# Kernel tuning notes

Hardware: AMD Instinct MI355X
Metric: run time of the kernel (lower is better)

Reference implementation:

```python
import jax, jax.numpy as jnp
import numpy as np

B, H, E_DIM, V = 512, 2048, 1024, 50257


def setup_inputs() -> dict:
    key = jax.random.key(0)
    ks = jax.random.split(key, 10)
    s_e = 1.0 / np.sqrt(E_DIM)
    s_h = 1.0 / np.sqrt(H)
    return {
        "inp": jax.random.randint(ks[0], (B,), 0, V),
        "h_0": jax.random.normal(ks[1], (B, H), jnp.float32) * 0.1,
        "c_0": jax.random.normal(ks[2], (B, H), jnp.float32) * 0.1,
        "E": jax.random.normal(ks[3], (V, E_DIM), jnp.float32),
        "Wx": jax.random.normal(ks[4], (4, H, E_DIM), jnp.float32) * s_e,
        "bx": jax.random.normal(ks[5], (4, H), jnp.float32) * s_e,
        "Wh": jax.random.normal(ks[6], (4, H, H), jnp.float32) * s_h,
        "bh": jax.random.normal(ks[7], (4, H), jnp.float32) * s_h,
        "Wd": jax.random.normal(ks[8], (V, H), jnp.float32) * s_h,
        "bd": jax.random.normal(ks[9], (V,), jnp.float32) * s_h,
    }


def reference(inp, h_0, c_0, E, Wx, bx, Wh, bh, Wd, bd):
    # Embedding lookup: [B, E_DIM]
    x = E[inp]
    # Two fused GEMMs for all 4 gates (gate order: f, i, o, c): [B, 4, H]
    gates = (jnp.einsum('be,ghe->bgh', x, Wx) + bx[None]
             + jnp.einsum('bh,gkh->bgk', h_0, Wh) + bh[None])
    f_g = jax.nn.sigmoid(gates[:, 0])
    i_g = jax.nn.sigmoid(gates[:, 1])
    o_g = jax.nn.sigmoid(gates[:, 2])
    c_tilda = jnp.tanh(gates[:, 3])
    cx = f_g * c_0 + i_g * c_tilda
    hx = o_g * jnp.tanh(cx)
    out = hx @ Wd.T + bd  # [B, V]
    return out, hx, cx
```

## Files before the change

### kernel.cpp

```cpp
#include <hip/hip_runtime.h>
#include <hip/hip_bf16.h>

using bf16x8 = __attribute__((ext_vector_type(8))) short;
using f32x4  = __attribute__((ext_vector_type(4))) float;

#define DEVI __device__ __forceinline__

DEVI unsigned short bf16r(float f)
{
    return __builtin_bit_cast(unsigned short, __float2bfloat16(f));
}

DEVI bf16x8 cvt8(const f32x4 a, const f32x4 b)
{
    bf16x8 r;
#pragma unroll
    for (int j = 0; j < 4; ++j) {
        r[j]     = (short)bf16r(a[j]);
        r[4 + j] = (short)bf16r(b[j]);
    }
    return r;
}

__global__ __launch_bounds__(256) void k_gather(const float* __restrict__ E,
                                                const int* __restrict__ inp,
                                                unsigned short* __restrict__ x)
{
    const int b = blockIdx.x;
    const long r = inp[b];
    const f32x4 v = ((const f32x4*)(E + r * 1024L))[threadIdx.x];
    ushort4 o;
    o.x = bf16r(v[0]); o.y = bf16r(v[1]); o.z = bf16r(v[2]); o.w = bf16r(v[3]);
    ((ushort4*)(x + (long)b * 1024L))[threadIdx.x] = o;
}

__global__ __launch_bounds__(256) void k_cvtn(const float* __restrict__ in,
                                              unsigned short* __restrict__ out)
{
    const long i = (blockIdx.x * 256L + threadIdx.x) * 8;
    const f32x4 a = *(const f32x4*)(in + i);
    const f32x4 b = *(const f32x4*)(in + i + 4);
    *(bf16x8*)(out + i) = cvt8(a, b);
}


DEVI bf16x8 lds_frag(const char* lds, int row, int j)
{
    return *(const bf16x8*)(lds + row * 128 + ((j ^ (row & 7)) << 4));
}

DEVI void mfma_tile8(const char* sA, const char* sB, int l, int wr, int wc,
                     f32x4 (&acc)[4][4])
{
#pragma unroll
    for (int ks = 0; ks < 2; ++ks) {
        bf16x8 af[4], bq[4];
#pragma unroll
        for (int m = 0; m < 4; ++m)
            af[m] = lds_frag(sA, wr * 64 + m * 16 + (l & 15), ks * 4 + (l >> 4));
#pragma unroll
        for (int n = 0; n < 4; ++n)
            bq[n] = lds_frag(sB, wc * 64 + n * 16 + (l & 15), ks * 4 + (l >> 4));
#pragma unroll
        for (int m = 0; m < 4; ++m)
#pragma unroll
            for (int n = 0; n < 4; ++n)
                acc[m][n] = __builtin_amdgcn_mfma_f32_16x16x32_bf16(
                    af[m], bq[n], acc[m][n], 0, 0, 0);
    }
}

template <bool CLAMP>
DEVI void gemm_core8(const unsigned short* __restrict__ A, long lda, long arow0,
                     const float* __restrict__ B, long ldb, long brow0, long bmax,
                     int nt, long kbase, int t, char* lds, f32x4 (&acc)[4][4])
{
    char* sA0 = lds;
    char* sA1 = lds + 32768;
    char* sB0 = lds + 65536;
    char* sB1 = lds + 81920;
    const int l = t & 63, w = t >> 6, wr = w >> 1, wc = w & 1;

    const unsigned short* ap[4];
    int aswz[4];
#pragma unroll
    for (int i = 0; i < 4; ++i) {
        const int g = i * 512 + t, row = g >> 3, j = g & 7;
        ap[i] = A + (arow0 + row) * lda + kbase + j * 8;
        aswz[i] = row * 128 + ((j ^ (row & 7)) << 4);
    }
    const float* bp[2];
    int bswz[2];
#pragma unroll
    for (int i = 0; i < 2; ++i) {
        const int g = i * 512 + t, row = g >> 3, j = g & 7;
        long br = brow0 + row;
        if (CLAMP) br = (br < bmax) ? br : (bmax - 1);
        bp[i] = B + br * ldb + kbase + j * 8;
        bswz[i] = row * 128 + ((j ^ (row & 7)) << 4);
    }

    bf16x8 ra0[4], ra1[4];
    f32x4 rb0[4], rb1[4];

#define LOADR(as, bs)                                                          \
    do {                                                                       \
        _Pragma("unroll") for (int i = 0; i < 4; ++i) {                        \
            as[i] = *(const bf16x8*)ap[i];                                     \
            ap[i] += 64;                                                       \
        }                                                                      \
        _Pragma("unroll") for (int i = 0; i < 2; ++i) {                        \
            bs[2 * i]     = *(const f32x4*)bp[i];                              \
            bs[2 * i + 1] = *(const f32x4*)(bp[i] + 4);                        \
            bp[i] += 64;                                                       \
        }                                                                      \
    } while (0)
#define WRLDS(sa, sb, as, bs)                                                  \
    do {                                                                       \
        _Pragma("unroll") for (int i = 0; i < 4; ++i)                          \
            *(bf16x8*)((sa) + aswz[i]) = as[i];                                \
        _Pragma("unroll") for (int i = 0; i < 2; ++i)                          \
            *(bf16x8*)((sb) + bswz[i]) = cvt8(bs[2 * i], bs[2 * i + 1]);       \
    } while (0)
#define WAITV8  asm volatile("s_waitcnt vmcnt(8)" ::: "memory")
#define WAITV0  asm volatile("s_waitcnt vmcnt(0)" ::: "memory")
#define WAITL0  asm volatile("s_waitcnt lgkmcnt(0)" ::: "memory")
#define BARRIER __builtin_amdgcn_s_barrier()

    LOADR(ra0, rb0);
    LOADR(ra1, rb1);
    WAITV8;
    WRLDS(sA0, sB0, ra0, rb0);
    LOADR(ra0, rb0);
    WAITL0; BARRIER;

    for (int kt = 0; kt < nt; kt += 2) {
        if (kt + 2 < nt) WAITV8; else WAITV0;
        WRLDS(sA1, sB1, ra1, rb1);
        if (kt + 3 < nt) LOADR(ra1, rb1);
        mfma_tile8(sA0, sB0, l, wr, wc, acc);
        WAITL0; BARRIER;
        if (kt + 2 < nt) {
            if (kt + 3 < nt) WAITV8; else WAITV0;
            WRLDS(sA0, sB0, ra0, rb0);
            if (kt + 4 < nt) LOADR(ra0, rb0);
        }
        mfma_tile8(sA1, sB1, l, wr, wc, acc);
        WAITL0; BARRIER;
    }
#undef LOADR
#undef WRLDS
#undef WAITV8
#undef WAITV0
#undef WAITL0
#undef BARRIER
}

__global__ __launch_bounds__(512, 2) void k_gates(
    const unsigned short* __restrict__ xb, const float* __restrict__ Wx,
    const unsigned short* __restrict__ h0b, const float* __restrict__ Wh,
    float* __restrict__ g0, float* __restrict__ g1, float* __restrict__ g2)
{
    extern __shared__ __align__(16) char lds[];
    const int t = threadIdx.x;
    const int bid = blockIdx.x;
    const int xcd = bid & 7, slot = bid >> 3;
    const int L = xcd * 48 + slot;
    const int z = L >> 7;
    const int mtile = L & 1;
    const int ntile = (L >> 1) & 63;

    const unsigned short* A; const float* B; long lda, ldb, kbase; float* C; int nt;
    if (z == 0)      { A = xb;  lda = 1024; B = Wx; ldb = 1024; kbase = 0;    C = g0; nt = 16; }
    else if (z == 1) { A = h0b; lda = 2048; B = Wh; ldb = 2048; kbase = 0;    C = g1; nt = 16; }
    else             { A = h0b; lda = 2048; B = Wh; ldb = 2048; kbase = 1024; C = g2; nt = 16; }

    f32x4 acc[4][4] = {};
    gemm_core8<false>(A, lda, (long)mtile * 256, B, ldb, (long)ntile * 128,
                      1L << 40, nt, kbase, t, lds, acc);

    const int l = t & 63, w = t >> 6, wr = w >> 1, wc = w & 1;
    const int lc = l & 15, r4 = (l >> 4) * 4;
#pragma unroll
    for (int n = 0; n < 4; ++n) {
        const long col = (long)ntile * 128 + wc * 64 + n * 16 + lc;
#pragma unroll
        for (int m = 0; m < 4; ++m) {
            const long row = (long)mtile * 256 + wr * 64 + m * 16 + r4;
#pragma unroll
            for (int r = 0; r < 4; ++r)
                C[(row + r) * 8192 + col] = acc[m][n][r];
        }
    }
}

__global__ __launch_bounds__(512, 2) void k_dec(
    const unsigned short* __restrict__ hxb, const float* __restrict__ Wd,
    const float* __restrict__ bd, float* __restrict__ out)
{
    extern __shared__ __align__(16) char lds[];
    const int t = threadIdx.x;
    const int bid = blockIdx.x;
    const int xcd = bid & 7, slot = bid >> 3;
    const int L = (xcd < 2) ? (xcd * 99 + slot) : (198 + (xcd - 2) * 98 + slot);
    const int mtile = L & 1;
    const int ntile = L >> 1;
    const long N = 50257;

    f32x4 acc[4][4] = {};
    gemm_core8<true>(hxb, 2048, (long)mtile * 256, Wd, 2048, (long)ntile * 128,
                     N, 32, 0, t, lds, acc);

    const int l = t & 63, w = t >> 6, wr = w >> 1, wc = w & 1;
    const int lc = l & 15, r4 = (l >> 4) * 4;
#pragma unroll
    for (int n = 0; n < 4; ++n) {
        const long col = (long)ntile * 128 + wc * 64 + n * 16 + lc;
        if (col >= N) continue;
        const float bias = bd[col];
#pragma unroll
        for (int m = 0; m < 4; ++m) {
            const long row = (long)mtile * 256 + wr * 64 + m * 16 + r4;
#pragma unroll
            for (int r = 0; r < 4; ++r)
                out[(row + r) * N + col] = acc[m][n][r] + bias;
        }
    }
}

__global__ __launch_bounds__(256) void k_lstm(
    const float* __restrict__ g0, const float* __restrict__ g1,
    const float* __restrict__ g2, const float* __restrict__ bx,
    const float* __restrict__ bh, const float* __restrict__ c0,
    float* __restrict__ hx, float* __restrict__ cx,
    unsigned short* __restrict__ hxb)
{
    const int i = blockIdx.x * 256 + threadIdx.x;
    const int b = i >> 9;
    const int hc = (i & 511) << 2;
    const long base = (long)b * 8192;

    f32x4 g[4];
#pragma unroll
    for (int gi = 0; gi < 4; ++gi) {
        const long off = base + gi * 2048 + hc;
        const int boff = gi * 2048 + hc;
        g[gi] = *(const f32x4*)(g0 + off);
        g[gi] += *(const f32x4*)(g1 + off);
        g[gi] += *(const f32x4*)(g2 + off);
        g[gi] += *(const f32x4*)(bx + boff);
        g[gi] += *(const f32x4*)(bh + boff);
    }
    const f32x4 c0v = *(const f32x4*)(c0 + (long)b * 2048 + hc);

    f32x4 cv, hv;
    ushort4 hb;
#pragma unroll
    for (int j = 0; j < 4; ++j) {
        const float fg = 1.f / (1.f + __expf(-g[0][j]));
        const float ig = 1.f / (1.f + __expf(-g[1][j]));
        const float og = 1.f / (1.f + __expf(-g[2][j]));
        const float e2 = __expf(2.f * g[3][j]);
        const float ct = 1.f - 2.f / (e2 + 1.f);
        const float c  = fg * c0v[j] + ig * ct;
        const float e2c = __expf(2.f * c);
        const float th  = 1.f - 2.f / (e2c + 1.f);
        cv[j] = c;
        hv[j] = og * th;
    }
    hb.x = bf16r(hv[0]); hb.y = bf16r(hv[1]); hb.z = bf16r(hv[2]); hb.w = bf16r(hv[3]);

    const long o = (long)b * 2048 + hc;
    *(f32x4*)(cx + o) = cv;
    *(f32x4*)(hx + o) = hv;
    *(ushort4*)(hxb + o) = hb;
}

extern "C" void kernel_launch(void* const* d_in, const int* in_sizes, int n_in,
                              void* d_out, int out_size, void* d_ws, size_t ws_size,
                              hipStream_t stream)
{
    const int*   inp = (const int*)d_in[0];
    const float* h0  = (const float*)d_in[1];
    const float* c0  = (const float*)d_in[2];
    const float* E   = (const float*)d_in[3];
    const float* Wx  = (const float*)d_in[4];
    const float* bx  = (const float*)d_in[5];
    const float* Wh  = (const float*)d_in[6];
    const float* bh  = (const float*)d_in[7];
    const float* Wd  = (const float*)d_in[8];
    const float* bd  = (const float*)d_in[9];

    float* out = (float*)d_out;
    float* hx  = out + 512L * 50257L;
    float* cx  = hx + 512L * 2048L;

    unsigned short* xb  = (unsigned short*)out;
    float* g0 = out + (1L << 20);
    float* g1 = out + (5L << 20);
    float* g2 = out + (9L << 20);
    unsigned short* h0b = (unsigned short*)(out + (13L << 20));
    unsigned short* hxb = (unsigned short*)d_ws;

    k_gather<<<512, 256, 0, stream>>>(E, inp, xb);
    k_cvtn<<<512, 256, 0, stream>>>(h0, h0b);

    k_gates<<<384, 512, 98304, stream>>>(xb, Wx, h0b, Wh, g0, g1, g2);

    k_lstm<<<1024, 256, 0, stream>>>(g0, g1, g2, bx, bh, c0, hx, cx, hxb);

    k_dec<<<786, 512, 98304, stream>>>(hxb, Wd, bd, out);
}
```

Baseline: 284.8 us.

## Use full-M 512-row tiles with K=32 steps so weights are read once

The GEMM core now covers all 512 batch rows in one block with 128 columns, using a K step of 32 instead of 64. Each weight row is therefore loaded from HBM and converted to bf16 only once, where before it was loaded twice across two M tiles. This roughly halves the dominant fp32 weight traffic for the decoder and gate GEMMs. The cost is half as many blocks (393 decoder blocks, 192 gate blocks), a larger accumulator that drops the two-blocks-per-CU launch bound, smaller K steps that double the number of barriers, and removal of the XCD-aware block remapping.

```diff
diff --git a/kernel.cpp b/kernel.cpp
--- a/kernel.cpp
+++ b/kernel.cpp
@@ -44,119 +44,109 @@
 }
 
 
-DEVI bf16x8 lds_frag(const char* lds, int row, int j)
-{
-    return *(const bf16x8*)(lds + row * 128 + ((j ^ (row & 7)) << 4));
-}
-
-DEVI void mfma_tile8(const char* sA, const char* sB, int l, int wr, int wc,
-                     f32x4 (&acc)[4][4])
-{
-#pragma unroll
-    for (int ks = 0; ks < 2; ++ks) {
-        bf16x8 af[4], bq[4];
-#pragma unroll
-        for (int m = 0; m < 4; ++m)
-            af[m] = lds_frag(sA, wr * 64 + m * 16 + (l & 15), ks * 4 + (l >> 4));
+DEVI void mfma_tile512(const char* sA, const char* sB, int l, int wr, int wc,
+                       f32x4 (&acc)[8][4])
+{
+    const int j = l >> 4;
+    bf16x8 af[8], bq[4];
+#pragma unroll
+    for (int m = 0; m < 8; ++m) {
+        const int row = wr * 128 + m * 16 + (l & 15);
+        af[m] = *(const bf16x8*)(sA + row * 64 + ((j ^ (row & 3)) << 4));
+    }
+#pragma unroll
+    for (int n = 0; n < 4; ++n) {
+        const int row = wc * 64 + n * 16 + (l & 15);
+        bq[n] = *(const bf16x8*)(sB + row * 64 + ((j ^ (row & 3)) << 4));
+    }
+#pragma unroll
+    for (int m = 0; m < 8; ++m)
 #pragma unroll
         for (int n = 0; n < 4; ++n)
-            bq[n] = lds_frag(sB, wc * 64 + n * 16 + (l & 15), ks * 4 + (l >> 4));
-#pragma unroll
-        for (int m = 0; m < 4; ++m)
-#pragma unroll
-            for (int n = 0; n < 4; ++n)
-                acc[m][n] = __builtin_amdgcn_mfma_f32_16x16x32_bf16(
-                    af[m], bq[n], acc[m][n], 0, 0, 0);
-    }
+            acc[m][n] = __builtin_amdgcn_mfma_f32_16x16x32_bf16(
+                af[m], bq[n], acc[m][n], 0, 0, 0);
 }
 
 template <bool CLAMP>
-DEVI void gemm_core8(const unsigned short* __restrict__ A, long lda, long arow0,
-                     const float* __restrict__ B, long ldb, long brow0, long bmax,
-                     int nt, long kbase, int t, char* lds, f32x4 (&acc)[4][4])
+DEVI void gemm_core512(const unsigned short* __restrict__ A, long lda,
+                       const float* __restrict__ B, long ldb, long bcol0,
+                       long bmax, int nt, long kbase, int t, char* lds,
+                       f32x4 (&acc)[8][4])
 {
     char* sA0 = lds;
     char* sA1 = lds + 32768;
     char* sB0 = lds + 65536;
-    char* sB1 = lds + 81920;
+    char* sB1 = lds + 73728;
     const int l = t & 63, w = t >> 6, wr = w >> 1, wc = w & 1;
 
     const unsigned short* ap[4];
     int aswz[4];
 #pragma unroll
     for (int i = 0; i < 4; ++i) {
-        const int g = i * 512 + t, row = g >> 3, j = g & 7;
-        ap[i] = A + (arow0 + row) * lda + kbase + j * 8;
-        aswz[i] = row * 128 + ((j ^ (row & 7)) << 4);
-    }
-    const float* bp[2];
-    int bswz[2];
-#pragma unroll
-    for (int i = 0; i < 2; ++i) {
-        const int g = i * 512 + t, row = g >> 3, j = g & 7;
-        long br = brow0 + row;
-        if (CLAMP) br = (br < bmax) ? br : (bmax - 1);
-        bp[i] = B + br * ldb + kbase + j * 8;
-        bswz[i] = row * 128 + ((j ^ (row & 7)) << 4);
-    }
+        const int g = i * 512 + t, row = g >> 2, j = g & 3;
+        ap[i] = A + row * lda + kbase + j * 8;
+        aswz[i] = row * 64 + ((j ^ (row & 3)) << 4);
+    }
+    const int brow = t >> 2, bseg = t & 3;
+    long br = bcol0 + brow;
+    if (CLAMP) br = (br < bmax) ? br : (bmax - 1);
+    const float* bp = B + br * ldb + kbase + bseg * 8;
+    const int bswz = brow * 64 + ((bseg ^ (brow & 3)) << 4);
 
     bf16x8 ra0[4], ra1[4];
-    f32x4 rb0[4], rb1[4];
+    f32x4 rb0[2], rb1[2];
 
 #define LOADR(as, bs)                                                          \
     do {                                                                       \
         _Pragma("unroll") for (int i = 0; i < 4; ++i) {                        \
             as[i] = *(const bf16x8*)ap[i];                                     \
-            ap[i] += 64;                                                       \
+            ap[i] += 32;                                                       \
         }                                                                      \
-        _Pragma("unroll") for (int i = 0; i < 2; ++i) {                        \
-            bs[2 * i]     = *(const f32x4*)bp[i];                              \
-            bs[2 * i + 1] = *(const f32x4*)(bp[i] + 4);                        \
-            bp[i] += 64;                                                       \
-        }                                                                      \
+        bs[0] = *(const f32x4*)bp;                                             \
+        bs[1] = *(const f32x4*)(bp + 4);                                       \
+        bp += 32;                                                              \
     } while (0)
 #define WRLDS(sa, sb, as, bs)                                                  \
     do {                                                                       \
         _Pragma("unroll") for (int i = 0; i < 4; ++i)                          \
             *(bf16x8*)((sa) + aswz[i]) = as[i];                                \
-        _Pragma("unroll") for (int i = 0; i < 2; ++i)                          \
-            *(bf16x8*)((sb) + bswz[i]) = cvt8(bs[2 * i], bs[2 * i + 1]);       \
+        *(bf16x8*)((sb) + bswz) = cvt8(bs[0], bs[1]);                          \
     } while (0)
-#define WAITV8  asm volatile("s_waitcnt vmcnt(8)" ::: "memory")
+#define WAITV6  asm volatile("s_waitcnt vmcnt(6)" ::: "memory")
 #define WAITV0  asm volatile("s_waitcnt vmcnt(0)" ::: "memory")
 #define WAITL0  asm volatile("s_waitcnt lgkmcnt(0)" ::: "memory")
 #define BARRIER __builtin_amdgcn_s_barrier()
 
     LOADR(ra0, rb0);
     LOADR(ra1, rb1);
-    WAITV8;
+    WAITV6;
     WRLDS(sA0, sB0, ra0, rb0);
     LOADR(ra0, rb0);
     WAITL0; BARRIER;
 
     for (int kt = 0; kt < nt; kt += 2) {
-        if (kt + 2 < nt) WAITV8; else WAITV0;
+        if (kt + 2 < nt) WAITV6; else WAITV0;
         WRLDS(sA1, sB1, ra1, rb1);
         if (kt + 3 < nt) LOADR(ra1, rb1);
-        mfma_tile8(sA0, sB0, l, wr, wc, acc);
+        mfma_tile512(sA0, sB0, l, wr, wc, acc);
         WAITL0; BARRIER;
         if (kt + 2 < nt) {
-            if (kt + 3 < nt) WAITV8; else WAITV0;
+            if (kt + 3 < nt) WAITV6; else WAITV0;
             WRLDS(sA0, sB0, ra0, rb0);
             if (kt + 4 < nt) LOADR(ra0, rb0);
         }
-        mfma_tile8(sA1, sB1, l, wr, wc, acc);
+        mfma_tile512(sA1, sB1, l, wr, wc, acc);
         WAITL0; BARRIER;
     }
 #undef LOADR
 #undef WRLDS
-#undef WAITV8
+#undef WAITV6
 #undef WAITV0
 #undef WAITL0
 #undef BARRIER
 }
 
-__global__ __launch_bounds__(512, 2) void k_gates(
+__global__ __launch_bounds__(512) void k_gates(
     const unsigned short* __restrict__ xb, const float* __restrict__ Wx,
     const unsigned short* __restrict__ h0b, const float* __restrict__ Wh,
     float* __restrict__ g0, float* __restrict__ g1, float* __restrict__ g2)
@@ -164,20 +154,17 @@
     extern __shared__ __align__(16) char lds[];
     const int t = threadIdx.x;
     const int bid = blockIdx.x;
-    const int xcd = bid & 7, slot = bid >> 3;
-    const int L = xcd * 48 + slot;
-    const int z = L >> 7;
-    const int mtile = L & 1;
-    const int ntile = (L >> 1) & 63;
-
-    const unsigned short* A; const float* B; long lda, ldb, kbase; float* C; int nt;
-    if (z == 0)      { A = xb;  lda = 1024; B = Wx; ldb = 1024; kbase = 0;    C = g0; nt = 16; }
-    else if (z == 1) { A = h0b; lda = 2048; B = Wh; ldb = 2048; kbase = 0;    C = g1; nt = 16; }
-    else             { A = h0b; lda = 2048; B = Wh; ldb = 2048; kbase = 1024; C = g2; nt = 16; }
-
-    f32x4 acc[4][4] = {};
-    gemm_core8<false>(A, lda, (long)mtile * 256, B, ldb, (long)ntile * 128,
-                      1L << 40, nt, kbase, t, lds, acc);
+    const int z = bid >> 6;
+    const int ntile = bid & 63;
+
+    const unsigned short* A; const float* B; long lda, ldb, kbase; float* C;
+    if (z == 0)      { A = xb;  lda = 1024; B = Wx; ldb = 1024; kbase = 0;    C = g0; }
+    else if (z == 1) { A = h0b; lda = 2048; B = Wh; ldb = 2048; kbase = 0;    C = g1; }
+    else             { A = h0b; lda = 2048; B = Wh; ldb = 2048; kbase = 1024; C = g2; }
+
+    f32x4 acc[8][4] = {};
+    gemm_core512<false>(A, lda, B, ldb, (long)ntile * 128, 1L << 40, 32, kbase,
+                        t, lds, acc);
 
     const int l = t & 63, w = t >> 6, wr = w >> 1, wc = w & 1;
     const int lc = l & 15, r4 = (l >> 4) * 4;
@@ -185,8 +172,8 @@
     for (int n = 0; n < 4; ++n) {
         const long col = (long)ntile * 128 + wc * 64 + n * 16 + lc;
 #pragma unroll
-        for (int m = 0; m < 4; ++m) {
-            const long row = (long)mtile * 256 + wr * 64 + m * 16 + r4;
+        for (int m = 0; m < 8; ++m) {
+            const long row = wr * 128 + m * 16 + r4;
 #pragma unroll
             for (int r = 0; r < 4; ++r)
                 C[(row + r) * 8192 + col] = acc[m][n][r];
@@ -194,22 +181,18 @@
     }
 }
 
-__global__ __launch_bounds__(512, 2) void k_dec(
+__global__ __launch_bounds__(512) void k_dec(
     const unsigned short* __restrict__ hxb, const float* __restrict__ Wd,
     const float* __restrict__ bd, float* __restrict__ out)
 {
     extern __shared__ __align__(16) char lds[];
     const int t = threadIdx.x;
-    const int bid = blockIdx.x;
-    const int xcd = bid & 7, slot = bid >> 3;
-    const int L = (xcd < 2) ? (xcd * 99 + slot) : (198 + (xcd - 2) * 98 + slot);
-    const int mtile = L & 1;
-    const int ntile = L >> 1;
+    const int ntile = blockIdx.x;
     const long N = 50257;
 
-    f32x4 acc[4][4] = {};
-    gemm_core8<true>(hxb, 2048, (long)mtile * 256, Wd, 2048, (long)ntile * 128,
-                     N, 32, 0, t, lds, acc);
+    f32x4 acc[8][4] = {};
+    gemm_core512<true>(hxb, 2048, Wd, 2048, (long)ntile * 128, N, 64, 0,
+                       t, lds, acc);
 
     const int l = t & 63, w = t >> 6, wr = w >> 1, wc = w & 1;
     const int lc = l & 15, r4 = (l >> 4) * 4;
@@ -219,8 +202,8 @@
         if (col >= N) continue;
         const float bias = bd[col];
 #pragma unroll
-        for (int m = 0; m < 4; ++m) {
-            const long row = (long)mtile * 256 + wr * 64 + m * 16 + r4;
+        for (int m = 0; m < 8; ++m) {
+            const long row = wr * 128 + m * 16 + r4;
 #pragma unroll
             for (int r = 0; r < 4; ++r)
                 out[(row + r) * N + col] = acc[m][n][r] + bias;
@@ -305,9 +288,9 @@
     k_gather<<<512, 256, 0, stream>>>(E, inp, xb);
     k_cvtn<<<512, 256, 0, stream>>>(h0, h0b);
 
-    k_gates<<<384, 512, 98304, stream>>>(xb, Wx, h0b, Wh, g0, g1, g2);
+    k_gates<<<192, 512, 81920, stream>>>(xb, Wx, h0b, Wh, g0, g1, g2);
 
     k_lstm<<<1024, 256, 0, stream>>>(g0, g1, g2, bx, bh, c0, hx, cx, hxb);
 
-    k_dec<<<786, 512, 98304, stream>>>(hxb, Wd, bd, out);
-}
+    k_dec<<<393, 512, 81920, stream>>>(hxb, Wd, bd, out);
+}
```

Result: slower. 290.8 us (+2.1%).
